# Kernel tuning notes

Hardware: AMD Instinct MI355X
Metric: run time of the kernel (lower is better)

## Reference

```python
import math
import jax, jax.numpy as jnp
import numpy as np

B, T, DIN, DH, E, TOPK = 2048, 512, 32, 96, 6, 2


def setup_inputs() -> dict:
    key = jax.random.key(0)
    ks = jax.random.split(key, 20)
    x = jax.random.normal(ks[0], (B, T, DIN), jnp.float32)
    lengths = jax.random.randint(ks[1], (B,), 1, T + 1)
    mask = (jnp.arange(T)[None, :] < lengths[:, None])

    def U(k, shape, fan):
        s = 1.0 / math.sqrt(fan)
        return jax.random.uniform(k, shape, jnp.float32, -s, s)

    # PyTorch LSTM init: U(-1/sqrt(DH), 1/sqrt(DH)); gate order i,f,g,o
    Wih = U(ks[2], (4 * DH, DIN), DH)
    Whh = U(ks[3], (4 * DH, DH), DH)
    bih = U(ks[4], (4 * DH,), DH)
    bhh = U(ks[5], (4 * DH,), DH)
    Wq = U(ks[6], (DH, DH), DH); bq = U(ks[7], (DH,), DH)
    Wk = U(ks[8], (DH, DH), DH); bk = U(ks[9], (DH,), DH)
    Wv = U(ks[10], (DH, DH), DH); bv = U(ks[11], (DH,), DH)
    Wg = U(ks[12], (E, 2 * DH), 2 * DH); bg = U(ks[13], (E,), 2 * DH)
    We1 = U(ks[14], (E, DH, 2 * DH), 2 * DH); be1 = U(ks[15], (E, DH), 2 * DH)
    We2 = U(ks[16], (E, DH), DH); be2 = U(ks[17], (E,), DH)
    return dict(x=x, lengths=lengths, mask=mask, Wih=Wih, Whh=Whh, bih=bih, bhh=bhh,
                Wq=Wq, bq=bq, Wk=Wk, bk=bk, Wv=Wv, bv=bv, Wg=Wg, bg=bg,
                We1=We1, be1=be1, We2=We2, be2=be2)


def _lstm(x, mask, Wih, Whh, bih, bhh):
    # packed-sequence semantics: carry frozen past each sample's length,
    # padded output positions zeroed (like pad_packed_sequence).
    xg = x @ Wih.T + bih  # [B,T,4*DH] precomputed input projection
    dh = Whh.shape[1]

    def step(carry, inp):
        h, c = carry
        xg_t, m_t = inp
        g = xg_t + h @ Whh.T + bhh
        i, f, gg, o = jnp.split(g, 4, axis=-1)
        c_new = jax.nn.sigmoid(f) * c + jax.nn.sigmoid(i) * jnp.tanh(gg)
        h_new = jax.nn.sigmoid(o) * jnp.tanh(c_new)
        m = m_t[:, None]
        h = jnp.where(m, h_new, h)
        c = jnp.where(m, c_new, c)
        return (h, c), jnp.where(m, h_new, 0.0)

    init = (jnp.zeros((x.shape[0], dh), x.dtype), jnp.zeros((x.shape[0], dh), x.dtype))
    (hT, _), H = jax.lax.scan(step, init, (jnp.swapaxes(xg, 0, 1), mask.T))
    return jnp.swapaxes(H, 0, 1), hT  # H:[B,T,DH], hT:[B,DH]


def reference(x, lengths, mask, Wih, Whh, bih, bhh, Wq, bq, Wk, bk, Wv, bv,
              Wg, bg, We1, be1, We2, be2):
    H, hT = _lstm(x, mask, Wih, Whh, bih, bhh)
    Q = hT @ Wq.T + bq                      # [B,DH]
    K = H @ Wk.T + bk                       # [B,T,DH]
    V = H @ Wv.T + bv                       # [B,T,DH]
    logits = jnp.einsum('bd,btd->bt', Q, K) / math.sqrt(K.shape[-1])
    logits = jnp.where(mask, logits, -1e9)
    alpha = jax.nn.softmax(logits, axis=1)  # [B,T]
    ctx = jnp.einsum('bt,btd->bd', alpha, V)
    feats = jnp.concatenate([ctx, hT], axis=-1)  # [B,2*DH]
    gate_logits = feats @ Wg.T + bg              # [B,E]
    topv, topi = jax.lax.top_k(gate_logits, TOPK)
    pi = jax.nn.softmax(topv, axis=-1)           # [B,TOPK]
    # all-expert dense compute (E tiny), then gather selected -> same math as
    # the per-expert masked scatter loop in the torch module (dropout off).
    h1 = jax.nn.relu(jnp.einsum('bf,ehf->beh', feats, We1) + be1[None])  # [B,E,DH]
    outs = jnp.einsum('beh,eh->be', h1, We2) + be2[None]                  # [B,E]
    sel = jnp.take_along_axis(outs, topi, axis=1)                         # [B,TOPK]
    yhat = jnp.sum(pi * sel, axis=-1, keepdims=True)                      # [B,1]
    return yhat, alpha, gate_logits
```

## Files before the change

kernel.cpp:

```cpp
#include <hip/hip_runtime.h>
#include <hip/hip_bf16.h>

#define B_ 2048
#define T_ 512
#define DIN_ 32
#define DH_ 96
#define NG_ 384
#define E_ 6

#define BPB 8
#define HP 104

typedef __attribute__((ext_vector_type(8))) _Float16 f16x8;
typedef __attribute__((ext_vector_type(4))) float f32x4;

#if defined(__has_builtin)
# if __has_builtin(__builtin_amdgcn_exp2f)
#  define EXP2F(x) __builtin_amdgcn_exp2f(x)
# endif
# if __has_builtin(__builtin_amdgcn_rcpf)
#  define RCPF(x) __builtin_amdgcn_rcpf(x)
# endif
#endif
#ifndef EXP2F
# define EXP2F(x) exp2f(x)
#endif
#ifndef RCPF
# define RCPF(x) (1.0f/(x))
#endif

__device__ __forceinline__ float sigf(float x) {
    return RCPF(1.0f + EXP2F(x * -1.44269504f));
}
__device__ __forceinline__ float tanhf_(float x) {
    return 1.0f - 2.0f * RCPF(1.0f + EXP2F(x * 2.88539008f));
}

__device__ __forceinline__ f16x8 cvt8(float4 a, float4 b) {
    f16x8 r;
    r[0] = (_Float16)a.x; r[1] = (_Float16)a.y; r[2] = (_Float16)a.z; r[3] = (_Float16)a.w;
    r[4] = (_Float16)b.x; r[5] = (_Float16)b.y; r[6] = (_Float16)b.z; r[7] = (_Float16)b.w;
    return r;
}
__device__ __forceinline__ f16x8 cvt8p(const float* p) {
    return cvt8(*(const float4*)p, *(const float4*)(p + 4));
}

__device__ __forceinline__ void lds_barrier() {
    asm volatile("s_waitcnt lgkmcnt(0)\n\ts_barrier" ::: "memory");
}

__global__ __launch_bounds__(768, 1) void lstm_kernel(
    const float* __restrict__ x, const int* __restrict__ lengths,
    const float* __restrict__ Wih, const float* __restrict__ Whh,
    const float* __restrict__ bih, const float* __restrict__ bhh,
    _Float16* __restrict__ Hout, float* __restrict__ hT)
{
    __shared__ float sgate[NG_ * 8];
    __shared__ _Float16 sh[2][16 * HP];

    const int tid  = threadIdx.x;
    const int bb   = blockIdx.x * BPB;
    const int wave = tid >> 6;
    const int lane = tid & 63;
    const int col  = lane & 15;
    const int quad = lane >> 4;

    int gc[2]; float bias[2];
    f16x8 wh[2][3], wi[2];
#pragma unroll
    for (int j = 0; j < 2; ++j) {
        const int tau = wave * 2 + j;
        const int g = tau / 6, u6 = tau % 6;
        const int gcj = g * DH_ + u6 * 16 + col;
        gc[j] = gcj;
#pragma unroll
        for (int kf = 0; kf < 3; ++kf)
            wh[j][kf] = cvt8p(Whh + gcj * DH_ + kf * 32 + quad * 8);
        wi[j] = cvt8p(Wih + gcj * DIN_ + quad * 8);
        bias[j] = bih[gcj] + bhh[gcj];
    }

    const int eu = tid >> 3;
    const int eb = tid & 7;
    float c1 = 0.f, hk1 = 0.f;
    const int len1 = lengths[bb + eb];

    const bool st_act = tid < 384;
    const int sb = tid / 48;
    const int su = (tid % 48) * 2;
    _Float16* Hst = Hout + ((long long)(bb + sb) * T_) * DH_ + su;

    const int xb = (bb + col < B_) ? (bb + col) : (B_ - 1);
    const float* xp = x + ((long long)xb * T_) * DIN_ + quad * 8;
    float4 xc0 = *(const float4*)xp;
    float4 xc1 = *(const float4*)(xp + 4);

    {
        _Float16* shf = &sh[0][0];
        for (int i = tid; i < 2 * 16 * HP; i += 768) shf[i] = (_Float16)0.f;
    }
    __syncthreads();

    for (int t = 0; t < T_; ++t) {
        const int buf = t & 1;

        const _Float16* hrow = &sh[buf][col * HP];
        f16x8 h0 = *(const f16x8*)(hrow + 0  + quad * 8);
        f16x8 h1 = *(const f16x8*)(hrow + 32 + quad * 8);
        f16x8 h2 = *(const f16x8*)(hrow + 64 + quad * 8);

        const float* xpn = (t + 1 < T_) ? (xp + DIN_) : xp;
        float4 xn0 = *(const float4*)xpn;
        float4 xn1 = *(const float4*)(xpn + 4);

        f16x8 xa = cvt8(xc0, xc1);

#pragma unroll
        for (int j = 0; j < 2; ++j) {
            f32x4 a = {bias[j], bias[j], bias[j], bias[j]};
            a = __builtin_amdgcn_mfma_f32_16x16x32_f16(h0, wh[j][0], a, 0, 0, 0);
            a = __builtin_amdgcn_mfma_f32_16x16x32_f16(h1, wh[j][1], a, 0, 0, 0);
            a = __builtin_amdgcn_mfma_f32_16x16x32_f16(h2, wh[j][2], a, 0, 0, 0);
            a = __builtin_amdgcn_mfma_f32_16x16x32_f16(xa, wi[j],    a, 0, 0, 0);
            if (quad < 2)
                *(f32x4*)&sgate[gc[j] * 8 + quad * 4] = a;
        }
        lds_barrier();

        {
            float iv = sgate[(0 * DH_ + eu) * 8 + eb];
            float fv = sgate[(1 * DH_ + eu) * 8 + eb];
            float gv = sgate[(2 * DH_ + eu) * 8 + eb];
            float ov = sgate[(3 * DH_ + eu) * 8 + eb];
            float cn = sigf(fv) * c1 + sigf(iv) * tanhf_(gv);
            float hn = sigf(ov) * tanhf_(cn);
            const bool m = t < len1;
            c1  = m ? cn : c1;
            hk1 = m ? hn : hk1;
            sh[buf ^ 1][eb * HP + eu] = (_Float16)hk1;
        }
        lds_barrier();

        if (st_act) {
            unsigned v = *(const unsigned*)&sh[buf ^ 1][sb * HP + su];
            *(unsigned*)Hst = v;
            Hst += DH_;
        }

        xp = xpn; xc0 = xn0; xc1 = xn1;
    }

    hT[(bb + eb) * DH_ + eu] = hk1;
}

__global__ __launch_bounds__(128) void qk_kernel(
    const float* __restrict__ hT, const float* __restrict__ Wq,
    const float* __restrict__ bq, const float* __restrict__ Wk,
    const float* __restrict__ bk, float* __restrict__ qk_out,
    float* __restrict__ qb_out)
{
    __shared__ float shT[DH_], sQ[DH_];
    const int b = blockIdx.x, tid = threadIdx.x;
    const float scale = 0.10206207262f;
    if (tid < DH_) shT[tid] = hT[b * DH_ + tid];
    __syncthreads();
    if (tid < DH_) {
        float acc = bq[tid];
        const float* wr = Wq + tid * DH_;
        for (int d = 0; d < DH_; d += 4) {
            float4 w4 = *(const float4*)(wr + d);
            acc += w4.x * shT[d] + w4.y * shT[d + 1] + w4.z * shT[d + 2] + w4.w * shT[d + 3];
        }
        sQ[tid] = acc;
    }
    __syncthreads();
    if (tid < DH_) {
        float acc = 0.f;
        for (int j = 0; j < DH_; ++j) acc += Wk[j * DH_ + tid] * sQ[j];
        qk_out[b * DH_ + tid] = acc * scale;
    }
    if (tid == 0) {
        float acc = 0.f;
        for (int d = 0; d < DH_; ++d) acc += sQ[d] * bk[d];
        qb_out[b] = acc * scale;
    }
}

__global__ __launch_bounds__(512) void attn_moe_kernel(
    const _Float16* __restrict__ H, const float* __restrict__ hT,
    const float* __restrict__ qk, const float* __restrict__ qb,
    const int* __restrict__ lengths,
    const float* __restrict__ Wv, const float* __restrict__ bv,
    const float* __restrict__ Wg, const float* __restrict__ bg,
    const float* __restrict__ We1, const float* __restrict__ be1,
    const float* __restrict__ We2, const float* __restrict__ be2,
    float* __restrict__ yhat_out, float* __restrict__ alpha_out,
    float* __restrict__ gl_out)
{
    __shared__ float salpha[T_];
    __shared__ float sqk[DH_];
    __shared__ float spart[4 * DH_];
    __shared__ float sfeats[2 * DH_];
    __shared__ float sh1[2][DH_];
    __shared__ float sred[8], ssum[8];
    __shared__ float sgl[E_];
    __shared__ float spi[2];
    __shared__ int stopi[2];

    const int b = blockIdx.x, tid = threadIdx.x;
    const int len = lengths[b];
    if (tid < DH_) sqk[tid] = qk[b * DH_ + tid];
    const float qbv = qb[b];
    __syncthreads();

    const _Float16* hr = H + ((long long)b * T_ + tid) * DH_;
    float l = qbv;
#pragma unroll
    for (int u = 0; u < DH_; u += 8) {
        f16x8 hv = *(const f16x8*)(hr + u);
        float4 qa = *(const float4*)&sqk[u];
        float4 qc = *(const float4*)&sqk[u + 4];
        l += (float)hv[0] * qa.x + (float)hv[1] * qa.y
           + (float)hv[2] * qa.z + (float)hv[3] * qa.w
           + (float)hv[4] * qc.x + (float)hv[5] * qc.y
           + (float)hv[6] * qc.z + (float)hv[7] * qc.w;
    }
    const bool valid = tid < len;
    float lv = valid ? l : -1e30f;

    float m = lv;
    for (int off = 32; off; off >>= 1) m = fmaxf(m, __shfl_xor(m, off));
    if ((tid & 63) == 0) sred[tid >> 6] = m;
    __syncthreads();
    m = sred[0];
#pragma unroll
    for (int i = 1; i < 8; ++i) m = fmaxf(m, sred[i]);

    float e = valid ? EXP2F((l - m) * 1.44269504f) : 0.f;
    float s = e;
    for (int off = 32; off; off >>= 1) s += __shfl_xor(s, off);
    if ((tid & 63) == 0) ssum[tid >> 6] = s;
    __syncthreads();
    s = ssum[0];
#pragma unroll
    for (int i = 1; i < 8; ++i) s += ssum[i];

    const float alpha = e * RCPF(s);
    salpha[tid] = alpha;
    alpha_out[(long long)b * T_ + tid] = alpha;
    __syncthreads();

    if (tid < 4 * DH_) {
        const int s4 = tid / DH_, u = tid - s4 * DH_;
        float acc = 0.f;
        const _Float16* hc = H + ((long long)b * T_) * DH_ + u;
        for (int t = s4 * 128; t < s4 * 128 + 128; ++t)
            acc += salpha[t] * (float)hc[t * DH_];
        spart[s4 * DH_ + u] = acc;
    }
    __syncthreads();
    if (tid < DH_) {
        float craw = spart[tid] + spart[DH_ + tid] + spart[2 * DH_ + tid] + spart[3 * DH_ + tid];
        spart[tid] = craw;
    }
    __syncthreads();
    if (tid < DH_) {
        float acc = bv[tid];
        const float* wr = Wv + tid * DH_;
        for (int u = 0; u < DH_; u += 4) {
            float4 w4 = *(const float4*)(wr + u);
            acc += w4.x * spart[u] + w4.y * spart[u + 1] + w4.z * spart[u + 2] + w4.w * spart[u + 3];
        }
        sfeats[tid] = acc;
        sfeats[DH_ + tid] = hT[b * DH_ + tid];
    }
    __syncthreads();

    if (tid < 192) {
        const int e6 = tid >> 5, cc = tid & 31;
        float p = 0.f;
        const float* wg = Wg + e6 * 2 * DH_;
#pragma unroll
        for (int j = 0; j < 6; ++j) p += wg[cc * 6 + j] * sfeats[cc * 6 + j];
        for (int off = 16; off; off >>= 1) p += __shfl_xor(p, off);
        if (cc == 0) {
            float g = p + bg[e6];
            sgl[e6] = g;
            gl_out[b * E_ + e6] = g;
        }
    }
    __syncthreads();

    if (tid == 0) {
        int i0 = 0; float v0 = sgl[0];
        for (int ee = 1; ee < E_; ++ee) if (sgl[ee] > v0) { v0 = sgl[ee]; i0 = ee; }
        int i1 = -1; float v1 = -1e30f;
        for (int ee = 0; ee < E_; ++ee) {
            if (ee == i0) continue;
            if (sgl[ee] > v1) { v1 = sgl[ee]; i1 = ee; }
        }
        float e1 = EXP2F((v1 - v0) * 1.44269504f);
        float inv = RCPF(1.f + e1);
        spi[0] = inv; spi[1] = e1 * inv;
        stopi[0] = i0; stopi[1] = i1;
    }
    __syncthreads();

    if (tid < 192) {
        const int e2 = tid / DH_, u = tid - e2 * DH_;
        const int ex = stopi[e2];
        float acc = be1[ex * DH_ + u];
        const float* w = We1 + ((long long)ex * DH_ + u) * (2 * DH_);
        for (int f = 0; f < 2 * DH_; f += 4) {
            float4 w4 = *(const float4*)(w + f);
            acc += w4.x * sfeats[f] + w4.y * sfeats[f + 1] + w4.z * sfeats[f + 2] + w4.w * sfeats[f + 3];
        }
        sh1[e2][u] = fmaxf(acc, 0.f);
    }
    __syncthreads();

    if (tid == 0) {
        float outs[2];
#pragma unroll
        for (int e2 = 0; e2 < 2; ++e2) {
            const int ex = stopi[e2];
            float a = be2[ex];
            for (int u = 0; u < DH_; ++u) a += sh1[e2][u] * We2[ex * DH_ + u];
            outs[e2] = a;
        }
        yhat_out[b] = spi[0] * outs[0] + spi[1] * outs[1];
    }
}

extern "C" void kernel_launch(void* const* d_in, const int* in_sizes, int n_in,
                              void* d_out, int out_size, void* d_ws, size_t ws_size,
                              hipStream_t stream) {
    const float* x   = (const float*)d_in[0];
    const int* lengths = (const int*)d_in[1];
    const float* Wih = (const float*)d_in[3];
    const float* Whh = (const float*)d_in[4];
    const float* bih = (const float*)d_in[5];
    const float* bhh = (const float*)d_in[6];
    const float* Wq  = (const float*)d_in[7];
    const float* bq  = (const float*)d_in[8];
    const float* Wk  = (const float*)d_in[9];
    const float* bk  = (const float*)d_in[10];
    const float* Wv  = (const float*)d_in[11];
    const float* bv  = (const float*)d_in[12];
    const float* Wg  = (const float*)d_in[13];
    const float* bg  = (const float*)d_in[14];
    const float* We1 = (const float*)d_in[15];
    const float* be1 = (const float*)d_in[16];
    const float* We2 = (const float*)d_in[17];
    const float* be2 = (const float*)d_in[18];

    float* yhat  = (float*)d_out;
    float* alpha = yhat + B_;
    float* gl    = alpha + (size_t)B_ * T_;

    char* ws = (char*)d_ws;
    _Float16* Hws = (_Float16*)ws;
    float* hTws = (float*)(ws + (size_t)B_ * T_ * DH_ * 2);
    float* qkws = hTws + (size_t)B_ * DH_;
    float* qbws = qkws + (size_t)B_ * DH_;

    lstm_kernel<<<dim3(B_ / BPB), dim3(768), 0, stream>>>(
        x, lengths, Wih, Whh, bih, bhh, Hws, hTws);
    qk_kernel<<<dim3(B_), dim3(128), 0, stream>>>(
        hTws, Wq, bq, Wk, bk, qkws, qbws);
    attn_moe_kernel<<<dim3(B_), dim3(512), 0, stream>>>(
        Hws, hTws, qkws, qbws, lengths, Wv, bv, Wg, bg,
        We1, be1, We2, be2, yhat, alpha, gl);
}
```

Baseline: 805.2 us.

## Concentrate LSTM gate MFMAs in eight waves and pad gate LDS stride

The recurrent gate matmuls now run on 8 of the 12 waves, with 3 gate tiles per wave instead of 2 tiles on every wave. The other 4 waves only do the elementwise cell update and the stores. The gate scratch buffer stride grows from 8 to 12 floats, which changes the LDS bank mapping for the gate writes and reads. The intent is to cut MFMA issue contention or LDS bank conflicts on the latency-bound recurrence. The cost is a longer serial MFMA chain per active wave and idle waves during the matmul phase.

```diff
diff --git a/kernel.cpp b/kernel.cpp
--- a/kernel.cpp
+++ b/kernel.cpp
@@ -10,6 +10,7 @@
 
 #define BPB 8
 #define HP 104
+#define GS 12
 
 typedef __attribute__((ext_vector_type(8))) _Float16 f16x8;
 typedef __attribute__((ext_vector_type(4))) float f32x4;
@@ -56,7 +57,7 @@
     const float* __restrict__ bih, const float* __restrict__ bhh,
     _Float16* __restrict__ Hout, float* __restrict__ hT)
 {
-    __shared__ float sgate[NG_ * 8];
+    __shared__ float sgate[NG_ * GS];
     __shared__ _Float16 sh[2][16 * HP];
 
     const int tid  = threadIdx.x;
@@ -65,20 +66,24 @@
     const int lane = tid & 63;
     const int col  = lane & 15;
     const int quad = lane >> 4;
-
-    int gc[2]; float bias[2];
-    f16x8 wh[2][3], wi[2];
-#pragma unroll
-    for (int j = 0; j < 2; ++j) {
-        const int tau = wave * 2 + j;
-        const int g = tau / 6, u6 = tau % 6;
-        const int gcj = g * DH_ + u6 * 16 + col;
-        gc[j] = gcj;
-#pragma unroll
-        for (int kf = 0; kf < 3; ++kf)
-            wh[j][kf] = cvt8p(Whh + gcj * DH_ + kf * 32 + quad * 8);
-        wi[j] = cvt8p(Wih + gcj * DIN_ + quad * 8);
-        bias[j] = bih[gcj] + bhh[gcj];
+    const bool mf  = wave < 8;
+
+    int gc[3] = {0, 0, 0};
+    float bias[3] = {0.f, 0.f, 0.f};
+    f16x8 wh[3][3], wi[3];
+    if (mf) {
+#pragma unroll
+        for (int j = 0; j < 3; ++j) {
+            const int tau = wave * 3 + j;
+            const int g = tau / 6, u6 = tau % 6;
+            const int gcj = g * DH_ + u6 * 16 + col;
+            gc[j] = gcj;
+#pragma unroll
+            for (int kf = 0; kf < 3; ++kf)
+                wh[j][kf] = cvt8p(Whh + gcj * DH_ + kf * 32 + quad * 8);
+            wi[j] = cvt8p(Wih + gcj * DIN_ + quad * 8);
+            bias[j] = bih[gcj] + bhh[gcj];
+        }
     }
 
     const int eu = tid >> 3;
@@ -93,8 +98,8 @@
 
     const int xb = (bb + col < B_) ? (bb + col) : (B_ - 1);
     const float* xp = x + ((long long)xb * T_) * DIN_ + quad * 8;
-    float4 xc0 = *(const float4*)xp;
-    float4 xc1 = *(const float4*)(xp + 4);
+    float4 xc0, xc1;
+    if (mf) { xc0 = *(const float4*)xp; xc1 = *(const float4*)(xp + 4); }
 
     {
         _Float16* shf = &sh[0][0];
@@ -105,34 +110,38 @@
     for (int t = 0; t < T_; ++t) {
         const int buf = t & 1;
 
-        const _Float16* hrow = &sh[buf][col * HP];
-        f16x8 h0 = *(const f16x8*)(hrow + 0  + quad * 8);
-        f16x8 h1 = *(const f16x8*)(hrow + 32 + quad * 8);
-        f16x8 h2 = *(const f16x8*)(hrow + 64 + quad * 8);
-
-        const float* xpn = (t + 1 < T_) ? (xp + DIN_) : xp;
-        float4 xn0 = *(const float4*)xpn;
-        float4 xn1 = *(const float4*)(xpn + 4);
-
-        f16x8 xa = cvt8(xc0, xc1);
-
-#pragma unroll
-        for (int j = 0; j < 2; ++j) {
-            f32x4 a = {bias[j], bias[j], bias[j], bias[j]};
-            a = __builtin_amdgcn_mfma_f32_16x16x32_f16(h0, wh[j][0], a, 0, 0, 0);
-            a = __builtin_amdgcn_mfma_f32_16x16x32_f16(h1, wh[j][1], a, 0, 0, 0);
-            a = __builtin_amdgcn_mfma_f32_16x16x32_f16(h2, wh[j][2], a, 0, 0, 0);
-            a = __builtin_amdgcn_mfma_f32_16x16x32_f16(xa, wi[j],    a, 0, 0, 0);
-            if (quad < 2)
-                *(f32x4*)&sgate[gc[j] * 8 + quad * 4] = a;
+        const float* xpn = xp;
+        if (mf) {
+            const _Float16* hrow = &sh[buf][col * HP];
+            f16x8 h0 = *(const f16x8*)(hrow + 0  + quad * 8);
+            f16x8 h1 = *(const f16x8*)(hrow + 32 + quad * 8);
+            f16x8 h2 = *(const f16x8*)(hrow + 64 + quad * 8);
+
+            xpn = (t + 1 < T_) ? (xp + DIN_) : xp;
+            float4 xn0 = *(const float4*)xpn;
+            float4 xn1 = *(const float4*)(xpn + 4);
+
+            f16x8 xa = cvt8(xc0, xc1);
+
+#pragma unroll
+            for (int j = 0; j < 3; ++j) {
+                f32x4 a = {bias[j], bias[j], bias[j], bias[j]};
+                a = __builtin_amdgcn_mfma_f32_16x16x32_f16(h0, wh[j][0], a, 0, 0, 0);
+                a = __builtin_amdgcn_mfma_f32_16x16x32_f16(h1, wh[j][1], a, 0, 0, 0);
+                a = __builtin_amdgcn_mfma_f32_16x16x32_f16(h2, wh[j][2], a, 0, 0, 0);
+                a = __builtin_amdgcn_mfma_f32_16x16x32_f16(xa, wi[j],    a, 0, 0, 0);
+                if (quad < 2)
+                    *(f32x4*)&sgate[gc[j] * GS + quad * 4] = a;
+            }
+            xc0 = xn0; xc1 = xn1;
         }
         lds_barrier();
 
         {
-            float iv = sgate[(0 * DH_ + eu) * 8 + eb];
-            float fv = sgate[(1 * DH_ + eu) * 8 + eb];
-            float gv = sgate[(2 * DH_ + eu) * 8 + eb];
-            float ov = sgate[(3 * DH_ + eu) * 8 + eb];
+            float iv = sgate[(0 * DH_ + eu) * GS + eb];
+            float fv = sgate[(1 * DH_ + eu) * GS + eb];
+            float gv = sgate[(2 * DH_ + eu) * GS + eb];
+            float ov = sgate[(3 * DH_ + eu) * GS + eb];
             float cn = sigf(fv) * c1 + sigf(iv) * tanhf_(gv);
             float hn = sigf(ov) * tanhf_(cn);
             const bool m = t < len1;
@@ -148,7 +157,7 @@
             Hst += DH_;
         }
 
-        xp = xpn; xc0 = xn0; xc1 = xn1;
+        xp = xpn;
     }
 
     hT[(bb + eb) * DH_ + eu] = hk1;
```

Measured after the change: 951.9 us. 18.2% more time.

## Sort sequences by length so LSTM blocks stop at their group's longest sequence

Applied to the files above, without the earlier changes.

Adds a small counting-sort pipeline (zero, count, scan, place) that builds a length-sorted permutation of the batch. Each LSTM block then processes 8 similar-length sequences and runs only up to their maximum length instead of all T steps. The H store is moved to right after the gate barrier, and the attention kernel skips loads and the context sum beyond each sequence's length. With one 768-thread block per CU and about as many blocks as CUs, the wall time may still be set by the longest-length blocks. The four extra tiny kernel launches add overhead.

```diff
diff --git a/kernel.cpp b/kernel.cpp
--- a/kernel.cpp
+++ b/kernel.cpp
@@ -10,6 +10,7 @@
 
 #define BPB 8
 #define HP 104
+#define GS 8
 
 typedef __attribute__((ext_vector_type(8))) _Float16 f16x8;
 typedef __attribute__((ext_vector_type(4))) float f32x4;
@@ -50,14 +51,46 @@
     asm volatile("s_waitcnt lgkmcnt(0)\n\ts_barrier" ::: "memory");
 }
 
+__global__ __launch_bounds__(512) void sort_zero_kernel(int* __restrict__ bins) {
+    bins[threadIdx.x] = 0;
+}
+__global__ __launch_bounds__(256) void sort_count_kernel(
+    const int* __restrict__ lengths, int* __restrict__ bins) {
+    const int b = blockIdx.x * 256 + threadIdx.x;
+    atomicAdd(&bins[lengths[b] - 1], 1);
+}
+__global__ __launch_bounds__(512) void sort_scan_kernel(
+    const int* __restrict__ bins, int* __restrict__ offs) {
+    __shared__ int s[512];
+    const int tid = threadIdx.x;
+    s[tid] = bins[tid];
+    __syncthreads();
+    for (int d = 1; d < 512; d <<= 1) {
+        int v = (tid >= d) ? s[tid - d] : 0;
+        __syncthreads();
+        s[tid] += v;
+        __syncthreads();
+    }
+    offs[tid] = s[tid] - bins[tid];
+}
+__global__ __launch_bounds__(256) void sort_place_kernel(
+    const int* __restrict__ lengths, int* __restrict__ offs,
+    int* __restrict__ perm) {
+    const int b = blockIdx.x * 256 + threadIdx.x;
+    const int pos = atomicAdd(&offs[lengths[b] - 1], 1);
+    perm[pos] = b;
+}
+
 __global__ __launch_bounds__(768, 1) void lstm_kernel(
     const float* __restrict__ x, const int* __restrict__ lengths,
+    const int* __restrict__ perm,
     const float* __restrict__ Wih, const float* __restrict__ Whh,
     const float* __restrict__ bih, const float* __restrict__ bhh,
     _Float16* __restrict__ Hout, float* __restrict__ hT)
 {
-    __shared__ float sgate[NG_ * 8];
+    __shared__ float sgate[NG_ * GS];
     __shared__ _Float16 sh[2][16 * HP];
+    __shared__ int sgb[BPB], slen[BPB];
 
     const int tid  = threadIdx.x;
     const int bb   = blockIdx.x * BPB;
@@ -66,6 +99,21 @@
     const int col  = lane & 15;
     const int quad = lane >> 4;
 
+    if (tid < BPB) {
+        const int g = perm[bb + tid];
+        sgb[tid] = g;
+        slen[tid] = lengths[g];
+    }
+    {
+        _Float16* shf = &sh[0][0];
+        for (int i = tid; i < 2 * 16 * HP; i += 768) shf[i] = (_Float16)0.f;
+    }
+    __syncthreads();
+
+    int bmax = slen[0];
+#pragma unroll
+    for (int i = 1; i < BPB; ++i) bmax = max(bmax, slen[i]);
+
     int gc[2]; float bias[2];
     f16x8 wh[2][3], wi[2];
 #pragma unroll
@@ -84,25 +132,18 @@
     const int eu = tid >> 3;
     const int eb = tid & 7;
     float c1 = 0.f, hk1 = 0.f;
-    const int len1 = lengths[bb + eb];
+    const int len1 = slen[eb];
 
     const bool st_act = tid < 384;
     const int sb = tid / 48;
     const int su = (tid % 48) * 2;
-    _Float16* Hst = Hout + ((long long)(bb + sb) * T_) * DH_ + su;
-
-    const int xb = (bb + col < B_) ? (bb + col) : (B_ - 1);
-    const float* xp = x + ((long long)xb * T_) * DIN_ + quad * 8;
+    _Float16* Hst = Hout + ((long long)sgb[sb] * T_) * DH_ + su;
+
+    const float* xp = x + ((long long)sgb[col & 7] * T_) * DIN_ + quad * 8;
     float4 xc0 = *(const float4*)xp;
     float4 xc1 = *(const float4*)(xp + 4);
 
-    {
-        _Float16* shf = &sh[0][0];
-        for (int i = tid; i < 2 * 16 * HP; i += 768) shf[i] = (_Float16)0.f;
-    }
-    __syncthreads();
-
-    for (int t = 0; t < T_; ++t) {
+    for (int t = 0; t < bmax; ++t) {
         const int buf = t & 1;
 
         const _Float16* hrow = &sh[buf][col * HP];
@@ -124,15 +165,21 @@
             a = __builtin_amdgcn_mfma_f32_16x16x32_f16(h2, wh[j][2], a, 0, 0, 0);
             a = __builtin_amdgcn_mfma_f32_16x16x32_f16(xa, wi[j],    a, 0, 0, 0);
             if (quad < 2)
-                *(f32x4*)&sgate[gc[j] * 8 + quad * 4] = a;
+                *(f32x4*)&sgate[gc[j] * GS + quad * 4] = a;
         }
         lds_barrier();
 
+        if (t > 0 && st_act) {
+            unsigned v = *(const unsigned*)&sh[buf][sb * HP + su];
+            *(unsigned*)Hst = v;
+            Hst += DH_;
+        }
+
         {
-            float iv = sgate[(0 * DH_ + eu) * 8 + eb];
-            float fv = sgate[(1 * DH_ + eu) * 8 + eb];
-            float gv = sgate[(2 * DH_ + eu) * 8 + eb];
-            float ov = sgate[(3 * DH_ + eu) * 8 + eb];
+            float iv = sgate[(0 * DH_ + eu) * GS + eb];
+            float fv = sgate[(1 * DH_ + eu) * GS + eb];
+            float gv = sgate[(2 * DH_ + eu) * GS + eb];
+            float ov = sgate[(3 * DH_ + eu) * GS + eb];
             float cn = sigf(fv) * c1 + sigf(iv) * tanhf_(gv);
             float hn = sigf(ov) * tanhf_(cn);
             const bool m = t < len1;
@@ -142,16 +189,15 @@
         }
         lds_barrier();
 
-        if (st_act) {
-            unsigned v = *(const unsigned*)&sh[buf ^ 1][sb * HP + su];
-            *(unsigned*)Hst = v;
-            Hst += DH_;
-        }
-
         xp = xpn; xc0 = xn0; xc1 = xn1;
     }
 
-    hT[(bb + eb) * DH_ + eu] = hk1;
+    if (st_act) {
+        unsigned v = *(const unsigned*)&sh[bmax & 1][sb * HP + su];
+        *(unsigned*)Hst = v;
+    }
+
+    hT[sgb[eb] * DH_ + eu] = hk1;
 }
 
 __global__ __launch_bounds__(128) void qk_kernel(
@@ -214,19 +260,21 @@
     const float qbv = qb[b];
     __syncthreads();
 
-    const _Float16* hr = H + ((long long)b * T_ + tid) * DH_;
+    const bool valid = tid < len;
     float l = qbv;
-#pragma unroll
-    for (int u = 0; u < DH_; u += 8) {
-        f16x8 hv = *(const f16x8*)(hr + u);
-        float4 qa = *(const float4*)&sqk[u];
-        float4 qc = *(const float4*)&sqk[u + 4];
-        l += (float)hv[0] * qa.x + (float)hv[1] * qa.y
-           + (float)hv[2] * qa.z + (float)hv[3] * qa.w
-           + (float)hv[4] * qc.x + (float)hv[5] * qc.y
-           + (float)hv[6] * qc.z + (float)hv[7] * qc.w;
-    }
-    const bool valid = tid < len;
+    if (valid) {
+        const _Float16* hr = H + ((long long)b * T_ + tid) * DH_;
+#pragma unroll
+        for (int u = 0; u < DH_; u += 8) {
+            f16x8 hv = *(const f16x8*)(hr + u);
+            float4 qa = *(const float4*)&sqk[u];
+            float4 qc = *(const float4*)&sqk[u + 4];
+            l += (float)hv[0] * qa.x + (float)hv[1] * qa.y
+               + (float)hv[2] * qa.z + (float)hv[3] * qa.w
+               + (float)hv[4] * qc.x + (float)hv[5] * qc.y
+               + (float)hv[6] * qc.z + (float)hv[7] * qc.w;
+        }
+    }
     float lv = valid ? l : -1e30f;
 
     float m = lv;
@@ -254,8 +302,9 @@
     if (tid < 4 * DH_) {
         const int s4 = tid / DH_, u = tid - s4 * DH_;
         float acc = 0.f;
+        const int t0 = s4 * 128, t1 = min(t0 + 128, len);
         const _Float16* hc = H + ((long long)b * T_) * DH_ + u;
-        for (int t = s4 * 128; t < s4 * 128 + 128; ++t)
+        for (int t = t0; t < t1; ++t)
             acc += salpha[t] * (float)hc[t * DH_];
         spart[s4 * DH_ + u] = acc;
     }
@@ -364,9 +413,17 @@
     float* hTws = (float*)(ws + (size_t)B_ * T_ * DH_ * 2);
     float* qkws = hTws + (size_t)B_ * DH_;
     float* qbws = qkws + (size_t)B_ * DH_;
+    int* bins   = (int*)(qbws + B_);
+    int* offs   = bins + 512;
+    int* perm   = offs + 512;
+
+    sort_zero_kernel<<<dim3(1), dim3(512), 0, stream>>>(bins);
+    sort_count_kernel<<<dim3(B_ / 256), dim3(256), 0, stream>>>(lengths, bins);
+    sort_scan_kernel<<<dim3(1), dim3(512), 0, stream>>>(bins, offs);
+    sort_place_kernel<<<dim3(B_ / 256), dim3(256), 0, stream>>>(lengths, offs, perm);
 
     lstm_kernel<<<dim3(B_ / BPB), dim3(768), 0, stream>>>(
-        x, lengths, Wih, Whh, bih, bhh, Hws, hTws);
+        x, lengths, perm, Wih, Whh, bih, bhh, Hws, hTws);
     qk_kernel<<<dim3(B_), dim3(128), 0, stream>>>(
         hTws, Wq, bq, Wk, bk, qkws, qbws);
     attn_moe_kernel<<<dim3(B_), dim3(512), 0, stream>>>(
```

Result: no change. 804.1 us (-0.1%).
